# Performance work log

Hardware: AMD Instinct MI355X
Metric: run time of the kernel (lower is better)

The kernel has to match this reference:

```python
import jax, jax.numpy as jnp
import numpy as np
import math

L = 8           # n_layers
DIM = 1024
H = 16          # num_heads
HD = DIM // H   # head_dim
HID = 4096      # mlp hidden
V = 32000       # vocab
B, T = 2, 1024


def setup_inputs() -> dict:
    key = jax.random.key(0)
    ks = jax.random.split(key, 10)
    s = 0.02
    inp = {
        "input_ids": jax.random.randint(ks[0], (B, T), 0, V, dtype=jnp.int32),
        "labels": jax.random.randint(ks[1], (B, T), 0, V, dtype=jnp.int32),
        "Wemb": jax.random.normal(ks[2], (V, DIM), jnp.float32) * s,   # tied embed / lm_head
        "Wq": jax.random.normal(ks[3], (L, DIM, DIM), jnp.float32) * s,
        "Wk": jax.random.normal(ks[4], (L, DIM, DIM), jnp.float32) * s,
        "Wv": jax.random.normal(ks[5], (L, DIM, DIM), jnp.float32) * s,
        "Wo": jax.random.normal(ks[6], (L, DIM, DIM), jnp.float32) * s,
        "Wfc": jax.random.normal(ks[7], (L, DIM, HID), jnp.float32) * s,
        "Wgate": jax.random.normal(ks[8], (L, DIM, HID), jnp.float32) * s,
        "Wproj": jax.random.normal(ks[9], (L, HID, DIM), jnp.float32) * s,
    }
    return inp


def _forward(input_ids, labels, Wemb, Wq, Wk, Wv, Wo, Wfc, Wgate, Wproj):
    b, t = input_ids.shape
    h = Wemb[input_ids]                                   # [B,T,C] embedding lookup
    # causal additive mask: -inf strictly above diagonal
    mask = jnp.triu(jnp.full((t, t), -jnp.inf, dtype=h.dtype), k=1)
    inv_sqrt_L = 1.0 / math.sqrt(L)
    inv_sqrt_hd = 1.0 / math.sqrt(HD)
    inv_sqrt_hid = 1.0 / math.sqrt(HID)

    def block(h, params):
        wq, wk, wv, wo, wfc, wgate, wproj = params
        # attention (explicit QK^T softmax V, as in source)
        q = (h @ wq).reshape(b, t, H, HD)
        k = (h @ wk).reshape(b, t, H, HD)
        v = (h @ wv).reshape(b, t, H, HD)
        scores = jnp.einsum("bqhd,bkhd->bhqk", q, k) * inv_sqrt_hd + mask
        probs = jax.nn.softmax(scores, axis=-1)
        attn = jnp.einsum("bhqk,bkhd->bqhd", probs, v).reshape(b, t, DIM)
        h = h + (attn @ wo) * inv_sqrt_L
        # SwiGLU MLP with 1/sqrt(hidden) scaling
        mlp = (((h @ wfc) * jax.nn.silu(h @ wgate)) * inv_sqrt_hid) @ wproj
        h = h + mlp * inv_sqrt_L
        return h, None

    h, _ = jax.lax.scan(block, h, (Wq, Wk, Wv, Wo, Wfc, Wgate, Wproj))

    logits = h @ Wemb.T                                   # tied lm_head [B,T,V]
    # cross entropy with ignore_index=-1
    lab = labels.reshape(-1)
    valid = lab != -1
    safe = jnp.where(valid, lab, 0)
    logp = jax.nn.log_softmax(logits.reshape(-1, V), axis=-1)
    nll = -jnp.take_along_axis(logp, safe[:, None], axis=-1)[:, 0]
    loss = jnp.sum(jnp.where(valid, nll, 0.0)) / jnp.maximum(jnp.sum(valid), 1)
    return logits, loss


def reference(input_ids, labels, Wemb, Wq, Wk, Wv, Wo, Wfc, Wgate, Wproj):
    return _forward(input_ids, labels, Wemb, Wq, Wk, Wv, Wo, Wfc, Wgate, Wproj)
```

## Files before the change

kernel.cpp:

```cpp
#include <hip/hip_runtime.h>
#include <hip/hip_bf16.h>
#include <math.h>

#define L_LAYERS 8
#define DIM 1024
#define NH 16
#define HD 64
#define HID 4096
#define VOCAB 32000
#define BB 2
#define TT 1024
#define MROWS (BB*TT)

typedef unsigned short u16;
typedef short short8 __attribute__((ext_vector_type(8)));
typedef float f32x4 __attribute__((ext_vector_type(4)));
typedef unsigned short us4 __attribute__((ext_vector_type(4)));
typedef unsigned short us8 __attribute__((ext_vector_type(8)));

__device__ __forceinline__ float bf2f(u16 x){
  union { unsigned int u; float f; } v; v.u = ((unsigned int)x) << 16; return v.f;
}
__device__ __forceinline__ u16 f2bf(float f){
  union { float f; unsigned int u; } v; v.f = f;
  unsigned int r = (v.u + 0x7fffu + ((v.u >> 16) & 1u)) >> 16; return (u16)r;
}

#define AS1 __attribute__((address_space(1)))
#define AS3 __attribute__((address_space(3)))
__device__ __forceinline__ void gld_lds16(const void* g, void* l){
  __builtin_amdgcn_global_load_lds((const AS1 void*)g, (AS3 void*)l, 16, 0, 0);
}

__global__ void k_embed(const int* __restrict__ ids, const float* __restrict__ Wemb,
                        float* __restrict__ h, u16* __restrict__ hb){
  int bt = blockIdx.x; long id = ids[bt];
  const float4* src = (const float4*)(Wemb + id*(long)DIM);
  float4 v = src[threadIdx.x];
  ((float4*)(h + (long)bt*DIM))[threadIdx.x] = v;
  us4 o = { f2bf(v.x), f2bf(v.y), f2bf(v.z), f2bf(v.w) };
  ((us4*)(hb + (long)bt*DIM))[threadIdx.x] = o;
}

__global__ void k_cvt(const float* __restrict__ src, u16* __restrict__ dst, long n){
  long i = ((long)blockIdx.x*256 + threadIdx.x)*8;
  if (i >= n) return;
  float4 a = ((const float4*)(src+i))[0];
  float4 b = ((const float4*)(src+i))[1];
  us4 o0 = { f2bf(a.x), f2bf(a.y), f2bf(a.z), f2bf(a.w) };
  us4 o1 = { f2bf(b.x), f2bf(b.y), f2bf(b.z), f2bf(b.w) };
  ((us4*)(dst+i))[0] = o0; ((us4*)(dst+i))[1] = o1;
}

__global__ void k_cvt_layer(const float* __restrict__ Wq, const float* __restrict__ Wk,
    const float* __restrict__ Wv, const float* __restrict__ Wo,
    const float* __restrict__ Wfc, const float* __restrict__ Wg, const float* __restrict__ Wp,
    u16* __restrict__ qkvT, u16* __restrict__ woT, u16* __restrict__ fgT, u16* __restrict__ projT)
{
  int tile = blockIdx.x;
  const float* src; u16* dst; int R, C, tr, tc;
  long rowmul = 1, rowoff = 0;
  if (tile < 1024){
    int m = tile >> 8, t2 = tile & 255;
    tr = t2 >> 4; tc = t2 & 15; R = 1024; C = 1024;
    src = (m==0)?Wq:(m==1)?Wk:(m==2)?Wv:Wo;
    dst = (m<3)? qkvT + (long)m*1024*1024 : woT;
  } else if (tile < 3072){
    int m = (tile - 1024) >> 10, t2 = (tile - 1024) & 1023;
    tr = t2 >> 6; tc = t2 & 63; R = 1024; C = 4096;
    src = m ? Wg : Wfc; dst = fgT; rowmul = 2; rowoff = m;
  } else {
    int t2 = tile - 3072;
    tr = t2 >> 4; tc = t2 & 15; R = 4096; C = 1024;
    src = Wp; dst = projT;
  }
  __shared__ float ls[64][65];
  int u = threadIdx.x, rr = u & 63, cc = u >> 6;
  const float* sp = src + (long)(tr*64 + rr)*C + tc*64 + cc*16;
  float4 v0 = ((const float4*)sp)[0];
  float4 v1 = ((const float4*)sp)[1];
  float4 v2 = ((const float4*)sp)[2];
  float4 v3 = ((const float4*)sp)[3];
  ls[rr][cc*16+ 0]=v0.x; ls[rr][cc*16+ 1]=v0.y; ls[rr][cc*16+ 2]=v0.z; ls[rr][cc*16+ 3]=v0.w;
  ls[rr][cc*16+ 4]=v1.x; ls[rr][cc*16+ 5]=v1.y; ls[rr][cc*16+ 6]=v1.z; ls[rr][cc*16+ 7]=v1.w;
  ls[rr][cc*16+ 8]=v2.x; ls[rr][cc*16+ 9]=v2.y; ls[rr][cc*16+10]=v2.z; ls[rr][cc*16+11]=v2.w;
  ls[rr][cc*16+12]=v3.x; ls[rr][cc*16+13]=v3.y; ls[rr][cc*16+14]=v3.z; ls[rr][cc*16+15]=v3.w;
  __syncthreads();
  int d  = u >> 2;
  int c4 = u & 3;
  long drow = (long)tc*64 + d;
  u16* dp = dst + (drow*rowmul + rowoff)*R + tr*64;
  #pragma unroll
  for (int g2 = 0; g2 < 2; ++g2){
    int e0 = (c4 + g2*4) * 8;
    us8 o;
    #pragma unroll
    for (int j=0;j<8;j++) o[j] = f2bf(ls[e0+j][d]);
    *((us8*)(dp + e0)) = o;
  }
}

template<int EPI>
__global__ __launch_bounds__(256, 2) void k_gemm(
    const u16* __restrict__ A, long lda,
    const u16* __restrict__ Bt, long ldb,
    void* __restrict__ Cp, long ldc,
    int K, int nMt, float alpha, int ksplit,
    u16* __restrict__ hbout)
{
  __shared__ u16 lsA[128*32];
  __shared__ u16 lsB[128*32];
  int nflat = gridDim.x; int w = blockIdx.x;
  if ((nflat & 7) == 0){ int q = nflat >> 3; w = (w & 7)*q + (w >> 3); }
  int perk = nflat / ksplit;
  int kc = w / perk; int w2 = w - kc*perk;
  int mtile = w2 % nMt, ntile = w2 / nMt;
  const u16* Ab = A + (long)mtile*128*lda + (long)kc*K;
  const u16* Bb = Bt + (long)ntile*128*ldb + (long)kc*K;
  int t = threadIdx.x;
  int wv = t >> 6, ln = t & 63;
  int srow = t >> 2;
  int scol = (t & 3) * 8;
  int fr = ln & 15, kg = ln >> 4;
  int wr = wv >> 1, wc = wv & 1;
  const f32x4 zero = {0.f,0.f,0.f,0.f};
  f32x4 acc[4][4];
  #pragma unroll
  for (int m=0;m<4;m++)
    #pragma unroll
    for (int n=0;n<4;n++) acc[m][n] = zero;
  const u16* ga0 = Ab + (long)srow*lda + scol;
  const u16* ga1 = Ab + (long)(srow+64)*lda + scol;
  const u16* gb0 = Bb + (long)srow*ldb + scol;
  const u16* gb1 = Bb + (long)(srow+64)*ldb + scol;
  u16* la0 = lsA + wv*512;
  u16* la1 = lsA + 2048 + wv*512;
  u16* lb0 = lsB + wv*512;
  u16* lb1 = lsB + 2048 + wv*512;
  for (int k0 = 0; k0 < K; k0 += 32){
    gld_lds16(ga0 + k0, la0);
    gld_lds16(ga1 + k0, la1);
    gld_lds16(gb0 + k0, lb0);
    gld_lds16(gb1 + k0, lb1);
    __syncthreads();
    short8 af[4], bfr[4];
    #pragma unroll
    for (int m=0;m<4;m++) af[m]  = *(const short8*)(lsA + (wr*64 + m*16 + fr)*32 + kg*8);
    #pragma unroll
    for (int n=0;n<4;n++) bfr[n] = *(const short8*)(lsB + (wc*64 + n*16 + fr)*32 + kg*8);
    #pragma unroll
    for (int m=0;m<4;m++)
      #pragma unroll
      for (int n=0;n<4;n++)
        acc[m][n] = __builtin_amdgcn_mfma_f32_16x16x32_bf16(af[m], bfr[n], acc[m][n], 0, 0, 0);
    __syncthreads();
  }
  long row0 = (long)mtile*128 + wr*64 + kg*4;
  int col0 = ntile*128 + wc*64 + fr;
  if constexpr (EPI == 0){
    u16* C = (u16*)Cp;
    #pragma unroll
    for (int m=0;m<4;m++)
      #pragma unroll
      for (int r=0;r<4;r++){
        long row = row0 + m*16 + r;
        #pragma unroll
        for (int n=0;n<4;n++) C[row*ldc + col0 + n*16] = f2bf(acc[m][n][r]);
      }
  } else if constexpr (EPI == 2){
    float* C = (float*)Cp;
    #pragma unroll
    for (int m=0;m<4;m++)
      #pragma unroll
      for (int r=0;r<4;r++){
        long row = row0 + m*16 + r;
        #pragma unroll
        for (int n=0;n<4;n++){
          long idx = row*ldc + col0 + n*16;
          float v = C[idx] + acc[m][n][r]*alpha;
          C[idx] = v;
          hbout[idx] = f2bf(v);
        }
      }
  } else {
    float* C = (float*)Cp + (long)kc*MROWS*ldc;
    #pragma unroll
    for (int m=0;m<4;m++)
      #pragma unroll
      for (int r=0;r<4;r++){
        long row = row0 + m*16 + r;
        #pragma unroll
        for (int n=0;n<4;n++) C[row*ldc + col0 + n*16] = acc[m][n][r];
      }
  }
}

__global__ void k_redK(const float* __restrict__ pK, float* __restrict__ h, u16* __restrict__ hb){
  long idx = ((long)blockIdx.x*256 + threadIdx.x)*4;
  const float aL = 0.35355339059327373f;
  float4 s0 = *(const float4*)(pK + idx);
  float4 s1 = *(const float4*)(pK + idx + (long)MROWS*1024);
  float4 s2 = *(const float4*)(pK + idx + (long)2*MROWS*1024);
  float4 s3 = *(const float4*)(pK + idx + (long)3*MROWS*1024);
  float4 hv = *(const float4*)(h + idx);
  float4 v;
  v.x = hv.x + (s0.x+s1.x+s2.x+s3.x)*aL;
  v.y = hv.y + (s0.y+s1.y+s2.y+s3.y)*aL;
  v.z = hv.z + (s0.z+s1.z+s2.z+s3.z)*aL;
  v.w = hv.w + (s0.w+s1.w+s2.w+s3.w)*aL;
  *(float4*)(h + idx) = v;
  us4 o = { f2bf(v.x), f2bf(v.y), f2bf(v.z), f2bf(v.w) };
  *(us4*)(hb + idx) = o;
}

#define MFMA_(va,vb,vc) __builtin_amdgcn_mfma_f32_16x16x32_bf16(va,vb,vc,0,0,0)
#define RDU(matofs, kt, kh, gr) (*(const short8*)(lds + \
      ((((kt)&1)*8 + (matofs) + (kh)*2 + ((gr)>>7))*4096) + \
      ((gr)&127)*32 + (((kg ^ (((gr)&3) ^ (((gr)>>2)&1))))<<3)))

template<int EPI>
__global__ __launch_bounds__(512, 1) void k_gemm256(
    const u16* __restrict__ A, long lda,
    const u16* __restrict__ Bt, long ldb,
    void* __restrict__ Cp, long ldc,
    int K, int nMt,
    float2* __restrict__ partials)
{
  __shared__ u16 lds[65536];
  int nwg = gridDim.x; int w = blockIdx.x;
  { int q = nwg >> 3, r8 = nwg & 7; int xcd = w & 7, lw = w >> 3;
    w = (xcd < r8 ? xcd*(q+1) : r8*(q+1) + (xcd-r8)*q) + lw; }
  int mtile = w % nMt, ntile = w / nMt;
  const u16* Abase = A + (long)mtile*256*lda;
  const u16* Bbase = Bt + (long)ntile*256*ldb;
  int tid = threadIdx.x;
  int wid = tid >> 6, ln = tid & 63;
  int wm = wid >> 2, wn = wid & 3;
  int fr = ln & 15, kg = ln >> 4;

  f32x4 acc[8][4];
  #pragma unroll
  for (int a=0;a<8;a++)
    #pragma unroll
    for (int b=0;b<4;b++) acc[a][b] = (f32x4){0.f,0.f,0.f,0.f};

  int sr_ = tid >> 2, sc_ = tid & 3;
  int ssw_ = (sr_ & 3) ^ ((sr_ >> 2) & 1);
  long sA0 = (long)sr_*lda + ((sc_ ^ ssw_) << 3);
  long sA1 = (long)(128 + sr_)*lda + ((sc_ ^ ssw_) << 3);
  long sB0 = (long)sr_*ldb + ((sc_ ^ ssw_) << 3);
  long sB1 = (long)(128 + sr_)*ldb + ((sc_ ^ ssw_) << 3);

#define STGGRP(kt, kh) do{ \
    int ub_ = ((kt)&1)*8 + (kh)*2; \
    long ko_ = ((long)(kt)<<6) + (kh)*32; \
    gld_lds16(Abase + sA0 + ko_, lds + (ub_+0)*4096 + (wid<<9)); \
    gld_lds16(Abase + sA1 + ko_, lds + (ub_+1)*4096 + (wid<<9)); \
    gld_lds16(Bbase + sB0 + ko_, lds + (ub_+4)*4096 + (wid<<9)); \
    gld_lds16(Bbase + sB1 + ko_, lds + (ub_+5)*4096 + (wid<<9)); \
  }while(0)

#define KBODY(kt, kh) do{ \
    short8 a0 = RDU(0, kt, kh, wm*128 +   0 + fr); \
    short8 a1 = RDU(0, kt, kh, wm*128 +  16 + fr); \
    short8 b0 = RDU(4, kt, kh, wn*64 +  0 + fr); \
    short8 b1 = RDU(4, kt, kh, wn*64 + 16 + fr); \
    short8 a2 = RDU(0, kt, kh, wm*128 +  32 + fr); \
    short8 a3 = RDU(0, kt, kh, wm*128 +  48 + fr); \
    short8 b2 = RDU(4, kt, kh, wn*64 + 32 + fr); \
    short8 b3 = RDU(4, kt, kh, wn*64 + 48 + fr); \
    short8 a4 = RDU(0, kt, kh, wm*128 +  64 + fr); \
    short8 a5 = RDU(0, kt, kh, wm*128 +  80 + fr); \
    short8 a6 = RDU(0, kt, kh, wm*128 +  96 + fr); \
    short8 a7 = RDU(0, kt, kh, wm*128 + 112 + fr); \
    __builtin_amdgcn_s_setprio(1); \
    acc[0][0]=MFMA_(a0,b0,acc[0][0]); acc[1][0]=MFMA_(a1,b0,acc[1][0]); \
    acc[0][1]=MFMA_(a0,b1,acc[0][1]); acc[1][1]=MFMA_(a1,b1,acc[1][1]); \
    acc[2][0]=MFMA_(a2,b0,acc[2][0]); acc[3][0]=MFMA_(a3,b0,acc[3][0]); \
    acc[2][1]=MFMA_(a2,b1,acc[2][1]); acc[3][1]=MFMA_(a3,b1,acc[3][1]); \
    acc[0][2]=MFMA_(a0,b2,acc[0][2]); acc[1][2]=MFMA_(a1,b2,acc[1][2]); \
    acc[0][3]=MFMA_(a0,b3,acc[0][3]); acc[1][3]=MFMA_(a1,b3,acc[1][3]); \
    acc[2][2]=MFMA_(a2,b2,acc[2][2]); acc[3][2]=MFMA_(a3,b2,acc[3][2]); \
    acc[2][3]=MFMA_(a2,b3,acc[2][3]); acc[3][3]=MFMA_(a3,b3,acc[3][3]); \
    acc[4][0]=MFMA_(a4,b0,acc[4][0]); acc[5][0]=MFMA_(a5,b0,acc[5][0]); \
    acc[4][1]=MFMA_(a4,b1,acc[4][1]); acc[5][1]=MFMA_(a5,b1,acc[5][1]); \
    acc[6][0]=MFMA_(a6,b0,acc[6][0]); acc[7][0]=MFMA_(a7,b0,acc[7][0]); \
    acc[6][1]=MFMA_(a6,b1,acc[6][1]); acc[7][1]=MFMA_(a7,b1,acc[7][1]); \
    acc[4][2]=MFMA_(a4,b2,acc[4][2]); acc[5][2]=MFMA_(a5,b2,acc[5][2]); \
    acc[4][3]=MFMA_(a4,b3,acc[4][3]); acc[5][3]=MFMA_(a5,b3,acc[5][3]); \
    acc[6][2]=MFMA_(a6,b2,acc[6][2]); acc[7][2]=MFMA_(a7,b2,acc[7][2]); \
    acc[6][3]=MFMA_(a6,b3,acc[6][3]); acc[7][3]=MFMA_(a7,b3,acc[7][3]); \
    __builtin_amdgcn_s_setprio(0); \
  }while(0)

  const int NT = K >> 6;
  STGGRP(0, 0);
  STGGRP(0, 1);
  if (NT > 1) STGGRP(1, 0);
  asm volatile("s_waitcnt vmcnt(8)" ::: "memory");

  for (int kt = 0; kt < NT; ++kt){
    __builtin_amdgcn_s_barrier();
    __builtin_amdgcn_sched_barrier(0);
    if (kt + 1 < NT){
      STGGRP(kt+1, 1);
      asm volatile("s_waitcnt vmcnt(12)" ::: "memory");
    } else {
      asm volatile("s_waitcnt vmcnt(4)" ::: "memory");
    }
    KBODY(kt, 0);
    __builtin_amdgcn_s_barrier();
    __builtin_amdgcn_sched_barrier(0);
    if (kt + 2 < NT){
      STGGRP(kt+2, 0);
      asm volatile("s_waitcnt vmcnt(12)" ::: "memory");
    } else if (kt + 1 < NT){
      asm volatile("s_waitcnt vmcnt(8)" ::: "memory");
    } else {
      asm volatile("s_waitcnt vmcnt(0)" ::: "memory");
    }
    KBODY(kt, 1);
  }

  if constexpr (EPI == 3){
    u16* act = (u16*)Cp;
    const float sc = 0.015625f;
    #pragma unroll
    for (int a=0;a<8;a++){
      long rowb = (long)mtile*256 + wm*128 + a*16 + kg*4;
      #pragma unroll
      for (int r=0;r<4;r++){
        #pragma unroll
        for (int b=0;b<4;b++){
          float v = acc[a][b][r];
          float pv = __shfl_xor(v, 1);
          if (!(fr & 1)){
            int colg = ntile*256 + wn*64 + b*16 + fr;
            float g = pv;
            float sl = g / (1.0f + __expf(-g));
            act[(rowb+r)*ldc + (colg>>1)] = f2bf(v * sl * sc);
          }
        }
      }
    }
  } else {
    float* C = (float*)Cp;
    #pragma unroll
    for (int a=0;a<8;a++){
      long rowb = (long)mtile*256 + wm*128 + a*16 + kg*4;
      #pragma unroll
      for (int r=0;r<4;r++){
        #pragma unroll
        for (int b=0;b<4;b++){
          int colg = ntile*256 + wn*64 + b*16 + fr;
          C[(rowb+r)*ldc + colg] = acc[a][b][r];
        }
      }
    }
    __syncthreads();
    float* pm = (float*)lds;
    float* ps = pm + 1024;
    #pragma unroll
    for (int a=0;a<8;a++)
      #pragma unroll
      for (int r=0;r<4;r++){
        float M = fmaxf(fmaxf(acc[a][0][r],acc[a][1][r]), fmaxf(acc[a][2][r],acc[a][3][r]));
        #pragma unroll
        for (int o=1;o<16;o<<=1) M = fmaxf(M, __shfl_xor(M, o));
        float S = __expf(acc[a][0][r]-M) + __expf(acc[a][1][r]-M)
                + __expf(acc[a][2][r]-M) + __expf(acc[a][3][r]-M);
        #pragma unroll
        for (int o=1;o<16;o<<=1) S += __shfl_xor(S, o);
        if (fr == 0){
          int rl = wm*128 + a*16 + kg*4 + r;
          pm[wn*256 + rl] = M; ps[wn*256 + rl] = S;
        }
      }
    __syncthreads();
    if (tid < 256){
      float m0 = pm[tid], m1 = pm[256+tid], m2 = pm[512+tid], m3 = pm[768+tid];
      float M = fmaxf(fmaxf(m0,m1), fmaxf(m2,m3));
      float S = ps[tid]*__expf(m0-M) + ps[256+tid]*__expf(m1-M)
              + ps[512+tid]*__expf(m2-M) + ps[768+tid]*__expf(m3-M);
      partials[((long)mtile*256 + tid)*128 + ntile] = make_float2(M, S);
    }
  }
#undef STGGRP
#undef KBODY
}

__global__ void k_transpose_v(const u16* __restrict__ qkv, u16* __restrict__ vT){
  int ttile = blockIdx.x; int z = blockIdx.y;
  long b = z >> 4; int hh = z & 15;
  const u16* v = qkv + b*TT*3072 + 2048 + hh*64;
  u16* outp = vT + (long)z*64*TT;
  __shared__ u16 ls[64][65];
  int u = threadIdx.x, rr = u & 63, cc = u >> 6;
  const u16* sp = v + (long)(ttile*64 + rr)*3072 + cc*16;
  us4 a0 = ((const us4*)sp)[0];
  us4 a1 = ((const us4*)sp)[1];
  us4 a2 = ((const us4*)sp)[2];
  us4 a3 = ((const us4*)sp)[3];
  #pragma unroll
  for (int j=0;j<4;j++){ ls[rr][cc*16+j] = a0[j]; ls[rr][cc*16+4+j] = a1[j];
                         ls[rr][cc*16+8+j] = a2[j]; ls[rr][cc*16+12+j] = a3[j]; }
  __syncthreads();
  int d = u & 63;
  #pragma unroll
  for (int g=0; g<4; ++g){
    int tl = cc*16 + g*4;
    int t  = ttile*64 + tl;
    int ut = (t >> 3) & 15;
    int tp = (t & ~127) + (((ut ^ (d & 15)) << 3) | (t & 7));
    us4 o = { ls[tl+0][d], ls[tl+1][d], ls[tl+2][d], ls[tl+3][d] };
    *((us4*)(outp + (long)d*TT + tp)) = o;
  }
}

__global__ __launch_bounds__(128) void k_flash(
    const u16* __restrict__ qkv, const u16* __restrict__ vT, u16* __restrict__ attnb)
{
  __shared__ u16 lsQ[64*64];
  __shared__ u16 lsK[128*64];
  __shared__ u16 lsV[64*128];
  __shared__ u16 lsP[64*128];
  int id = blockIdx.x;
  int wq = id >> 5, z = id & 31;
  int qt = (wq < 8) ? wq : 23 - wq;
  long bT = (long)(z >> 4) * TT;
  int h64 = (z & 15) * 64;
  int t = threadIdx.x, wv = t >> 6, ln = t & 63;
  int fr = ln & 15, kg = ln >> 4;
  const u16* vbase = vT + (long)z*64*TT;

  #pragma unroll
  for (int p=0; p<4; ++p){
    int r = p*16 + wv*8 + (ln>>3);
    const u16* g = qkv + (bT + qt*64 + r)*3072 + h64 + (((ln&7) ^ (ln>>3))*8);
    gld_lds16(g, lsQ + (p*16 + wv*8)*64);
  }

  f32x4 S[2][8], O[2][4];
  float Mst[2][4], Lst[2][4];
  #pragma unroll
  for (int m=0;m<2;m++){
    #pragma unroll
    for (int n=0;n<4;n++) O[m][n] = (f32x4){0.f,0.f,0.f,0.f};
    #pragma unroll
    for (int r=0;r<4;r++){ Mst[m][r] = -3.0e38f; Lst[m][r] = 0.f; }
  }

  int nk = (qt >> 1) + 1;
  for (int kt = 0; kt < nk; ++kt){
    #pragma unroll
    for (int p=0; p<8; ++p){
      int r = p*16 + wv*8 + (ln>>3);
      const u16* g = qkv + (bT + kt*128 + r)*3072 + 1024 + h64 + (((ln&7) ^ (ln>>3))*8);
      gld_lds16(g, lsK + (p*16 + wv*8)*64);
    }
    #pragma unroll
    for (int p=0; p<8; ++p){
      int d = p*8 + wv*4 + (ln>>4);
      const u16* g = vbase + (long)d*TT + kt*128 + (ln&15)*8;
      gld_lds16(g, lsV + (p*8 + wv*4)*128);
    }
    __syncthreads();

    #pragma unroll
    for (int m=0;m<2;m++)
      #pragma unroll
      for (int n=0;n<8;n++) S[m][n] = (f32x4){0.f,0.f,0.f,0.f};
    #pragma unroll
    for (int ks=0; ks<2; ++ks){
      int un = ((ks*4 + kg) ^ (fr & 7)) * 8;
      short8 a0 = *(const short8*)(lsQ + (wv*32 +      fr)*64 + un);
      short8 a1 = *(const short8*)(lsQ + (wv*32 + 16 + fr)*64 + un);
      #pragma unroll
      for (int n=0;n<8;n++){
        short8 bb = *(const short8*)(lsK + (n*16 + fr)*64 + un);
        S[0][n] = __builtin_amdgcn_mfma_f32_16x16x32_bf16(a0, bb, S[0][n], 0,0,0);
        S[1][n] = __builtin_amdgcn_mfma_f32_16x16x32_bf16(a1, bb, S[1][n], 0,0,0);
      }
    }

    #pragma unroll
    for (int m=0;m<2;m++){
      #pragma unroll
      for (int r=0;r<4;r++){
        int rloc = wv*32 + m*16 + kg*4 + r;
        int row_g = qt*64 + rloc;
        float x[8]; float mx = -3.0e38f;
        #pragma unroll
        for (int n=0;n<8;n++){
          int col_g = kt*128 + n*16 + fr;
          x[n] = (col_g <= row_g) ? S[m][n][r]*0.125f : -3.0e38f;
          mx = fmaxf(mx, x[n]);
        }
        #pragma unroll
        for (int o=1;o<16;o<<=1) mx = fmaxf(mx, __shfl_xor(mx, o));
        float Mnew = fmaxf(Mst[m][r], mx);
        float corr = __expf(Mst[m][r] - Mnew);
        Mst[m][r] = Mnew;
        float s = 0.f;
        #pragma unroll
        for (int n=0;n<8;n++){
          float p = __expf(x[n] - Mnew);
          s += p;
          int col = n*16 + fr;
          int col2 = ((((col>>3) ^ (rloc & 15)) << 3) | (col & 7));
          lsP[rloc*128 + col2] = f2bf(p);
        }
        #pragma unroll
        for (int o=1;o<16;o<<=1) s += __shfl_xor(s, o);
        Lst[m][r] = Lst[m][r]*corr + s;
        #pragma unroll
        for (int n=0;n<4;n++) O[m][n][r] *= corr;
      }
    }

    #pragma unroll
    for (int ks=0; ks<4; ++ks){
      int up = ((ks*4 + kg) ^ fr) * 8;
      short8 p0 = *(const short8*)(lsP + (wv*32 +      fr)*128 + up);
      short8 p1 = *(const short8*)(lsP + (wv*32 + 16 + fr)*128 + up);
      #pragma unroll
      for (int n=0;n<4;n++){
        short8 vb = *(const short8*)(lsV + (n*16 + fr)*128 + up);
        O[0][n] = __builtin_amdgcn_mfma_f32_16x16x32_bf16(p0, vb, O[0][n], 0,0,0);
        O[1][n] = __builtin_amdgcn_mfma_f32_16x16x32_bf16(p1, vb, O[1][n], 0,0,0);
      }
    }
    __syncthreads();
  }

  #pragma unroll
  for (int m=0;m<2;m++)
    #pragma unroll
    for (int r=0;r<4;r++){
      float inv = 1.0f / Lst[m][r];
      long row = bT + qt*64 + wv*32 + m*16 + kg*4 + r;
      #pragma unroll
      for (int n=0;n<4;n++)
        attnb[row*1024 + h64 + n*16 + fr] = f2bf(O[m][n][r]*inv);
    }
}

__global__ void k_nll2(const float2* __restrict__ part, const float* __restrict__ logits,
                       const int* __restrict__ labels, float* __restrict__ nll){
  int row = blockIdx.x; int ln = threadIdx.x;
  const float2* pr = part + (long)row*128;
  float m = -3.0e38f, s = 0.f;
  for (int j = ln; j < 125; j += 64){
    float2 p = pr[j];
    float M = fmaxf(m, p.x);
    s = s*__expf(m - M) + p.y*__expf(p.x - M);
    m = M;
  }
  #pragma unroll
  for (int o=32;o;o>>=1){
    float om = __shfl_xor(m, o), os = __shfl_xor(s, o);
    float M = fmaxf(m, om);
    s = s*__expf(m - M) + os*__expf(om - M);
    m = M;
  }
  if (ln == 0){
    int lab = labels[row];
    float lse = m + __logf(s);
    nll[row] = (lab != -1) ? (lse - logits[(long)row*VOCAB + lab]) : 0.f;
  }
}

__global__ void k_loss(const float* __restrict__ nll, const int* __restrict__ labels,
                       float* __restrict__ out){
  int tid = threadIdx.x;
  int wv = tid >> 6;
  float s = 0.f; float c = 0.f;
  for (int i = tid; i < MROWS; i += 256){
    s += nll[i];
    c += (labels[i] != -1) ? 1.f : 0.f;
  }
  #pragma unroll
  for (int o=32;o;o>>=1){ s += __shfl_xor(s, o); c += __shfl_xor(c, o); }
  __shared__ float rsm[4], rc[4];
  if ((tid & 63) == 0){ rsm[wv] = s; rc[wv] = c; }
  __syncthreads();
  if (tid == 0){
    s = rsm[0]+rsm[1]+rsm[2]+rsm[3];
    c = rc[0]+rc[1]+rc[2]+rc[3];
    out[(long)MROWS*VOCAB] = s / fmaxf(c, 1.f);
  }
}

extern "C" void kernel_launch(void* const* d_in, const int* in_sizes, int n_in,
                              void* d_out, int out_size, void* d_ws, size_t ws_size,
                              hipStream_t stream)
{
  (void)in_sizes; (void)n_in; (void)out_size; (void)ws_size;
  const int*   ids    = (const int*)d_in[0];
  const int*   labels = (const int*)d_in[1];
  const float* Wemb   = (const float*)d_in[2];
  const float* Wq     = (const float*)d_in[3];
  const float* Wk     = (const float*)d_in[4];
  const float* Wv     = (const float*)d_in[5];
  const float* Wo     = (const float*)d_in[6];
  const float* Wfc    = (const float*)d_in[7];
  const float* Wg     = (const float*)d_in[8];
  const float* Wp     = (const float*)d_in[9];
  float* logits = (float*)d_out;

  char* ws = (char*)d_ws;
  size_t off = 0;
  auto alloc = [&](size_t bytes){ void* p = ws + off; off += (bytes + 255) & ~(size_t)255; return p; };
  u16*    wembBf = (u16*)alloc((size_t)VOCAB*DIM*2);
  float*  h      = (float*)alloc((size_t)MROWS*DIM*4);
  u16*    hb     = (u16*)alloc((size_t)MROWS*DIM*2);
  u16*    qkvT   = (u16*)alloc((size_t)3*DIM*DIM*2);
  u16*    woT    = (u16*)alloc((size_t)DIM*DIM*2);
  u16*    fgT    = (u16*)alloc((size_t)2*HID*DIM*2);
  u16*    projT  = (u16*)alloc((size_t)DIM*HID*2);
  u16*    qkv    = (u16*)alloc((size_t)MROWS*3*DIM*2);
  u16*    vT     = (u16*)alloc((size_t)BB*NH*64*TT*2);
  u16*    attnb  = (u16*)alloc((size_t)MROWS*DIM*2);
  u16*    act    = (u16*)alloc((size_t)MROWS*HID*2);
  float*  pK     = (float*)alloc((size_t)4*MROWS*DIM*4);
  float2* parts  = (float2*)alloc((size_t)MROWS*128*8);
  float*  nllb   = (float*)alloc((size_t)MROWS*4);

  dim3 blk(256,1,1);
  dim3 blk512(512,1,1);
  const float aL = 0.35355339059327373f;

  k_cvt<<<dim3(16000,1,1),blk,0,stream>>>(Wemb, wembBf, (long)VOCAB*DIM);
  k_embed<<<dim3(MROWS,1,1),blk,0,stream>>>(ids, Wemb, h, hb);

  for (int l = 0; l < L_LAYERS; ++l){
    k_cvt_layer<<<dim3(4096,1,1),blk,0,stream>>>(
        Wq + (size_t)l*DIM*DIM, Wk + (size_t)l*DIM*DIM, Wv + (size_t)l*DIM*DIM, Wo + (size_t)l*DIM*DIM,
        Wfc + (size_t)l*DIM*HID, Wg + (size_t)l*DIM*HID, Wp + (size_t)l*HID*DIM,
        qkvT, woT, fgT, projT);
    k_gemm<0><<<dim3(384,1,1),blk,0,stream>>>(hb,1024, qkvT,1024, qkv,3072,
        1024,16,1.f,1, nullptr);
    k_transpose_v<<<dim3(16,32,1),blk,0,stream>>>(qkv, vT);
    k_flash<<<dim3(512,1,1),dim3(128,1,1),0,stream>>>(qkv, vT, attnb);
    k_gemm<2><<<dim3(128,1,1),blk,0,stream>>>(attnb,1024, woT,1024, h,1024,
        1024,16,aL,1, hb);
    k_gemm256<3><<<dim3(256,1,1),blk512,0,stream>>>(hb,1024, fgT,1024, act,4096,
        1024,8, nullptr);
    k_gemm<5><<<dim3(512,1,1),blk,0,stream>>>(act,4096, projT,4096, pK,1024,
        1024,16,1.f,4, nullptr);
    k_redK<<<dim3(2048,1,1),blk,0,stream>>>(pK, h, hb);
  }
  k_gemm256<4><<<dim3(1000,1,1),blk512,0,stream>>>(hb,1024, wembBf,1024, logits,32000,
      1024,8, parts);
  k_nll2<<<dim3(MROWS,1,1),dim3(64,1,1),0,stream>>>(parts, logits, labels, nllb);
  k_loss<<<dim3(1,1,1),blk,0,stream>>>(nllb, labels, logits);
}
```

Measured before the change: 1.917 ms.

## Restructure 256x256 GEMM main loop into eight-phase ping-pong schedule

Rewrites the k_gemm256 mainloop as a two-iteration unrolled schedule of eight phases. Each phase loads half the A fragments plus the B fragments from LDS, issues one staged global-to-LDS load, then runs 16 MFMAs between paired barriers. The goal is to interleave LDS reads, global prefetch and MFMA work more evenly and cut register pressure from holding all A fragments at once. It also drops the __syncthreads before the epilogue's LDS reuse, relying on the loop's trailing barrier. This adds many more barriers per K step, and it assumes NT is even (K divisible by 128).

```diff
diff --git a/kernel.cpp b/kernel.cpp
--- a/kernel.cpp
+++ b/kernel.cpp
@@ -214,9 +214,60 @@
 }
 
 #define MFMA_(va,vb,vc) __builtin_amdgcn_mfma_f32_16x16x32_bf16(va,vb,vc,0,0,0)
-#define RDU(matofs, kt, kh, gr) (*(const short8*)(lds + \
-      ((((kt)&1)*8 + (matofs) + (kh)*2 + ((gr)>>7))*4096) + \
-      ((gr)&127)*32 + (((kg ^ (((gr)&3) ^ (((gr)>>2)&1))))<<3)))
+#define RDS(dbf, isB, khh, R0) \
+  (*(const short8*)((const u16*)lds + ((((dbf)<<2)+((isB)<<1)+(khh))<<13) + (R0)*32 + kuo))
+#define STG(isB, khh, dbf, kt) do{ \
+    const u16* sb_ = (isB) ? Bbase : Abase; \
+    long sld_ = (isB) ? ldb : lda; \
+    long sko_ = ((long)(kt)<<6) + ((khh)<<5); \
+    u16* sd_ = (u16*)lds + ((long)(((dbf)<<2) + ((isB)<<1) + (khh))<<13) + (wid<<9); \
+    gld_lds16(sb_ + (long)sr0*sld_ + suo + sko_, sd_); \
+    gld_lds16(sb_ + (long)(sr0+128)*sld_ + suo + sko_, sd_ + 4096); \
+  }while(0)
+#define MM16(o) do{ \
+    acc[(o)+0][0]=MFMA_(va0,vb0,acc[(o)+0][0]); \
+    acc[(o)+1][0]=MFMA_(va1,vb0,acc[(o)+1][0]); \
+    acc[(o)+2][0]=MFMA_(va2,vb0,acc[(o)+2][0]); \
+    acc[(o)+3][0]=MFMA_(va3,vb0,acc[(o)+3][0]); \
+    acc[(o)+0][1]=MFMA_(va0,vb1,acc[(o)+0][1]); \
+    acc[(o)+1][1]=MFMA_(va1,vb1,acc[(o)+1][1]); \
+    acc[(o)+2][1]=MFMA_(va2,vb1,acc[(o)+2][1]); \
+    acc[(o)+3][1]=MFMA_(va3,vb1,acc[(o)+3][1]); \
+    acc[(o)+0][2]=MFMA_(va0,vb2,acc[(o)+0][2]); \
+    acc[(o)+1][2]=MFMA_(va1,vb2,acc[(o)+1][2]); \
+    acc[(o)+2][2]=MFMA_(va2,vb2,acc[(o)+2][2]); \
+    acc[(o)+3][2]=MFMA_(va3,vb2,acc[(o)+3][2]); \
+    acc[(o)+0][3]=MFMA_(va0,vb3,acc[(o)+0][3]); \
+    acc[(o)+1][3]=MFMA_(va1,vb3,acc[(o)+1][3]); \
+    acc[(o)+2][3]=MFMA_(va2,vb3,acc[(o)+2][3]); \
+    acc[(o)+3][3]=MFMA_(va3,vb3,acc[(o)+3][3]); \
+  }while(0)
+#define PH(dbf, khh, half, DOSTG, SisB, Skh, Sdbf, Skt, WAITK) do{ \
+    va0 = RDS(dbf, 0, khh, wm*128 + (half)*64 +  0); \
+    va1 = RDS(dbf, 0, khh, wm*128 + (half)*64 + 16); \
+    va2 = RDS(dbf, 0, khh, wm*128 + (half)*64 + 32); \
+    va3 = RDS(dbf, 0, khh, wm*128 + (half)*64 + 48); \
+    if (!(half)){ \
+      vb0 = RDS(dbf, 1, khh, wn*64 +  0); \
+      vb1 = RDS(dbf, 1, khh, wn*64 + 16); \
+      vb2 = RDS(dbf, 1, khh, wn*64 + 32); \
+      vb3 = RDS(dbf, 1, khh, wn*64 + 48); \
+    } \
+    if (DOSTG) STG(SisB, Skh, Sdbf, Skt); \
+    if (WAITK){ \
+      if (DOSTG) asm volatile("s_waitcnt vmcnt(4)" ::: "memory"); \
+      else       asm volatile("s_waitcnt vmcnt(0)" ::: "memory"); \
+    } \
+    __builtin_amdgcn_sched_barrier(0); \
+    __builtin_amdgcn_s_barrier(); \
+    asm volatile("s_waitcnt lgkmcnt(0)" ::: "memory"); \
+    __builtin_amdgcn_sched_barrier(0); \
+    __builtin_amdgcn_s_setprio(1); \
+    MM16((half)*4); \
+    __builtin_amdgcn_s_setprio(0); \
+    __builtin_amdgcn_sched_barrier(0); \
+    __builtin_amdgcn_s_barrier(); \
+  }while(0)
 
 template<int EPI>
 __global__ __launch_bounds__(512, 1) void k_gemm256(
@@ -237,89 +288,44 @@
   int wid = tid >> 6, ln = tid & 63;
   int wm = wid >> 2, wn = wid & 3;
   int fr = ln & 15, kg = ln >> 4;
+  int swfr = (fr & 3) ^ ((fr >> 2) & 1);
+  int kuo = fr*32 + ((kg ^ swfr) << 3);
+  int sr0 = tid >> 2;
+  int ssw = (sr0 & 3) ^ ((sr0 >> 2) & 1);
+  long suo = (long)(((tid & 3) ^ ssw) << 3);
 
   f32x4 acc[8][4];
   #pragma unroll
   for (int a=0;a<8;a++)
     #pragma unroll
     for (int b=0;b<4;b++) acc[a][b] = (f32x4){0.f,0.f,0.f,0.f};
-
-  int sr_ = tid >> 2, sc_ = tid & 3;
-  int ssw_ = (sr_ & 3) ^ ((sr_ >> 2) & 1);
-  long sA0 = (long)sr_*lda + ((sc_ ^ ssw_) << 3);
-  long sA1 = (long)(128 + sr_)*lda + ((sc_ ^ ssw_) << 3);
-  long sB0 = (long)sr_*ldb + ((sc_ ^ ssw_) << 3);
-  long sB1 = (long)(128 + sr_)*ldb + ((sc_ ^ ssw_) << 3);
-
-#define STGGRP(kt, kh) do{ \
-    int ub_ = ((kt)&1)*8 + (kh)*2; \
-    long ko_ = ((long)(kt)<<6) + (kh)*32; \
-    gld_lds16(Abase + sA0 + ko_, lds + (ub_+0)*4096 + (wid<<9)); \
-    gld_lds16(Abase + sA1 + ko_, lds + (ub_+1)*4096 + (wid<<9)); \
-    gld_lds16(Bbase + sB0 + ko_, lds + (ub_+4)*4096 + (wid<<9)); \
-    gld_lds16(Bbase + sB1 + ko_, lds + (ub_+5)*4096 + (wid<<9)); \
-  }while(0)
-
-#define KBODY(kt, kh) do{ \
-    short8 a0 = RDU(0, kt, kh, wm*128 +   0 + fr); \
-    short8 a1 = RDU(0, kt, kh, wm*128 +  16 + fr); \
-    short8 b0 = RDU(4, kt, kh, wn*64 +  0 + fr); \
-    short8 b1 = RDU(4, kt, kh, wn*64 + 16 + fr); \
-    short8 a2 = RDU(0, kt, kh, wm*128 +  32 + fr); \
-    short8 a3 = RDU(0, kt, kh, wm*128 +  48 + fr); \
-    short8 b2 = RDU(4, kt, kh, wn*64 + 32 + fr); \
-    short8 b3 = RDU(4, kt, kh, wn*64 + 48 + fr); \
-    short8 a4 = RDU(0, kt, kh, wm*128 +  64 + fr); \
-    short8 a5 = RDU(0, kt, kh, wm*128 +  80 + fr); \
-    short8 a6 = RDU(0, kt, kh, wm*128 +  96 + fr); \
-    short8 a7 = RDU(0, kt, kh, wm*128 + 112 + fr); \
-    __builtin_amdgcn_s_setprio(1); \
-    acc[0][0]=MFMA_(a0,b0,acc[0][0]); acc[1][0]=MFMA_(a1,b0,acc[1][0]); \
-    acc[0][1]=MFMA_(a0,b1,acc[0][1]); acc[1][1]=MFMA_(a1,b1,acc[1][1]); \
-    acc[2][0]=MFMA_(a2,b0,acc[2][0]); acc[3][0]=MFMA_(a3,b0,acc[3][0]); \
-    acc[2][1]=MFMA_(a2,b1,acc[2][1]); acc[3][1]=MFMA_(a3,b1,acc[3][1]); \
-    acc[0][2]=MFMA_(a0,b2,acc[0][2]); acc[1][2]=MFMA_(a1,b2,acc[1][2]); \
-    acc[0][3]=MFMA_(a0,b3,acc[0][3]); acc[1][3]=MFMA_(a1,b3,acc[1][3]); \
-    acc[2][2]=MFMA_(a2,b2,acc[2][2]); acc[3][2]=MFMA_(a3,b2,acc[3][2]); \
-    acc[2][3]=MFMA_(a2,b3,acc[2][3]); acc[3][3]=MFMA_(a3,b3,acc[3][3]); \
-    acc[4][0]=MFMA_(a4,b0,acc[4][0]); acc[5][0]=MFMA_(a5,b0,acc[5][0]); \
-    acc[4][1]=MFMA_(a4,b1,acc[4][1]); acc[5][1]=MFMA_(a5,b1,acc[5][1]); \
-    acc[6][0]=MFMA_(a6,b0,acc[6][0]); acc[7][0]=MFMA_(a7,b0,acc[7][0]); \
-    acc[6][1]=MFMA_(a6,b1,acc[6][1]); acc[7][1]=MFMA_(a7,b1,acc[7][1]); \
-    acc[4][2]=MFMA_(a4,b2,acc[4][2]); acc[5][2]=MFMA_(a5,b2,acc[5][2]); \
-    acc[4][3]=MFMA_(a4,b3,acc[4][3]); acc[5][3]=MFMA_(a5,b3,acc[5][3]); \
-    acc[6][2]=MFMA_(a6,b2,acc[6][2]); acc[7][2]=MFMA_(a7,b2,acc[7][2]); \
-    acc[6][3]=MFMA_(a6,b3,acc[6][3]); acc[7][3]=MFMA_(a7,b3,acc[7][3]); \
-    __builtin_amdgcn_s_setprio(0); \
-  }while(0)
+  short8 va0,va1,va2,va3, vb0,vb1,vb2,vb3;
 
   const int NT = K >> 6;
-  STGGRP(0, 0);
-  STGGRP(0, 1);
-  if (NT > 1) STGGRP(1, 0);
-  asm volatile("s_waitcnt vmcnt(8)" ::: "memory");
-
-  for (int kt = 0; kt < NT; ++kt){
-    __builtin_amdgcn_s_barrier();
-    __builtin_amdgcn_sched_barrier(0);
-    if (kt + 1 < NT){
-      STGGRP(kt+1, 1);
-      asm volatile("s_waitcnt vmcnt(12)" ::: "memory");
-    } else {
-      asm volatile("s_waitcnt vmcnt(4)" ::: "memory");
-    }
-    KBODY(kt, 0);
-    __builtin_amdgcn_s_barrier();
-    __builtin_amdgcn_sched_barrier(0);
-    if (kt + 2 < NT){
-      STGGRP(kt+2, 0);
-      asm volatile("s_waitcnt vmcnt(12)" ::: "memory");
-    } else if (kt + 1 < NT){
-      asm volatile("s_waitcnt vmcnt(8)" ::: "memory");
-    } else {
-      asm volatile("s_waitcnt vmcnt(0)" ::: "memory");
-    }
-    KBODY(kt, 1);
+  STG(0,0,0, 0);
+  STG(1,0,0, 0);
+  STG(0,1,0, 0);
+  STG(1,1,0, 0);
+  if (NT > 1){
+    STG(0,0,1, 1);
+    STG(1,0,1, 1);
+    asm volatile("s_waitcnt vmcnt(4)" ::: "memory");
+  } else {
+    asm volatile("s_waitcnt vmcnt(0)" ::: "memory");
+  }
+  __builtin_amdgcn_s_barrier();
+
+  #pragma unroll 1
+  for (int jt = 0; jt < NT; jt += 2){
+    int s2 = (jt+2 < NT), s3 = (jt+3 < NT);
+    PH(0,0,0, 1,  0,1,1, jt+1, 0);
+    PH(0,0,1, 1,  1,1,1, jt+1, 0);
+    PH(0,1,0, s2, 0,0,0, jt+2, 0);
+    PH(0,1,1, s2, 1,0,0, jt+2, 1);
+    PH(1,0,0, s2, 0,1,0, jt+2, 0);
+    PH(1,0,1, s2, 1,1,0, jt+2, 0);
+    PH(1,1,0, s3, 0,0,1, jt+3, 0);
+    PH(1,1,1, s3, 1,0,1, jt+3, 1);
   }
 
   if constexpr (EPI == 3){
@@ -357,7 +363,6 @@
         }
       }
     }
-    __syncthreads();
     float* pm = (float*)lds;
     float* ps = pm + 1024;
     #pragma unroll
@@ -385,8 +390,6 @@
       partials[((long)mtile*256 + tid)*128 + ntile] = make_float2(M, S);
     }
   }
-#undef STGGRP
-#undef KBODY
 }
 
 __global__ void k_transpose_v(const u16* __restrict__ qkv, u16* __restrict__ vT){
```

New measurement: 1.908 ms. About the same (-0.5%).
